# Optimization experiments

Hardware: AMD Instinct MI355X
Metric: run time of the kernel (lower is better)

The kernel has to match this reference:

```python
import jax, jax.numpy as jnp
import numpy as np

T, BLOCK, SIG = 4096, 1024, 1024
LAM = 0.25


def _lstm_cell(x, h, c, Wih, Whh, bih, bhh):
    # PyTorch LSTM gate order: i, f, g, o
    gates = x @ Wih.T + h @ Whh.T + bih + bhh  # [1, 4H]
    i, f, g, o = jnp.split(gates, 4, axis=-1)
    i = jax.nn.sigmoid(i)
    f = jax.nn.sigmoid(f)
    g = jnp.tanh(g)
    o = jax.nn.sigmoid(o)
    c_new = f * c + i * g
    h_new = o * jnp.tanh(c_new)
    return h_new, c_new


def setup_inputs() -> dict:
    key = jax.random.key(0)
    ks = jax.random.split(key, 9)
    ke = 1.0 / np.sqrt(SIG)
    kd = 1.0 / np.sqrt(BLOCK)
    inputs = jax.random.normal(ks[0], (T, 1, BLOCK), dtype=jnp.float32)
    enc_Wih = jax.random.uniform(ks[1], (4 * SIG, BLOCK), jnp.float32, -ke, ke)
    enc_Whh = jax.random.uniform(ks[2], (4 * SIG, SIG), jnp.float32, -ke, ke)
    enc_bih = jax.random.uniform(ks[3], (4 * SIG,), jnp.float32, -ke, ke)
    enc_bhh = jax.random.uniform(ks[4], (4 * SIG,), jnp.float32, -ke, ke)
    dec_Wih = jax.random.uniform(ks[5], (4 * BLOCK, SIG), jnp.float32, -kd, kd)
    dec_Whh = jax.random.uniform(ks[6], (4 * BLOCK, BLOCK), jnp.float32, -kd, kd)
    dec_bih = jax.random.uniform(ks[7], (4 * BLOCK,), jnp.float32, -kd, kd)
    dec_bhh = jax.random.uniform(ks[8], (4 * BLOCK,), jnp.float32, -kd, kd)
    return {"inputs": inputs, "enc_Wih": enc_Wih, "enc_Whh": enc_Whh,
            "enc_bih": enc_bih, "enc_bhh": enc_bhh, "dec_Wih": dec_Wih,
            "dec_Whh": dec_Whh, "dec_bih": dec_bih, "dec_bhh": dec_bhh}


def reference(inputs, enc_Wih, enc_Whh, enc_bih, enc_bhh,
              dec_Wih, dec_Whh, dec_bih, dec_bhh):
    H = enc_Whh.shape[1]
    B = inputs.shape[-1]

    # encode: full-sequence LSTM, zero initial state, batch=1
    def enc_step(carry, x):
        h, c = carry
        h, c = _lstm_cell(x, h, c, enc_Wih, enc_Whh, enc_bih, enc_bhh)
        return (h, c), h

    h0 = jnp.zeros((1, H), inputs.dtype)
    c0 = jnp.zeros((1, H), inputs.dtype)
    _, signal = jax.lax.scan(enc_step, (h0, c0), inputs)  # [T, 1, H]

    # decode: one LSTM step per i; h0 reset to inputs[i], cell state carried
    def dec_step(c, xs):
        x, h_init = xs  # x = signal[i+1], h_init = inputs[i]
        h, c = _lstm_cell(x, h_init, c, dec_Wih, dec_Whh, dec_bih, dec_bhh)
        return c, h

    cdec0 = jnp.zeros((1, B), inputs.dtype)
    _, decoded = jax.lax.scan(dec_step, cdec0, (signal[1:], inputs[:-1]))  # [T-1, 1, B]

    target = inputs[1:]
    mse_loss = jnp.mean((decoded - target) ** 2)
    l1_reg = jnp.sum(jnp.abs(signal)) / signal.size
    loss = mse_loss + LAM * l1_reg
    return loss, mse_loss, l1_reg
```

## Files before the change

kernel.cpp:

```cpp
#include <hip/hip_runtime.h>
#include <math.h>

#define TSTEPS 4096
#define DIM 1024
#define GDIM 4096
#define ENC_NB 64
#define NREP 8
#define NSEG 64
#define SEGLEN 64

typedef short bf16x8 __attribute__((ext_vector_type(8)));
typedef float f32x4 __attribute__((ext_vector_type(4)));
typedef unsigned int uint4v __attribute__((ext_vector_type(4)));

__device__ __forceinline__ float sigmoidf_(float x) {
    return 1.0f / (1.0f + expf(-x));
}

__device__ __forceinline__ void loadcvt(const float* __restrict__ p,
                                        bf16x8& hi, bf16x8& lo)
{
    float4 a = *(const float4*)p;
    float4 b = *(const float4*)(p + 4);
    float f[8] = {a.x, a.y, a.z, a.w, b.x, b.y, b.z, b.w};
    uint4v hw, lw;
    #pragma unroll
    for (int j = 0; j < 4; ++j) {
        unsigned u0 = __float_as_uint(f[2*j]);
        unsigned u1 = __float_as_uint(f[2*j+1]);
        unsigned m0 = u0 & 0xffff0000u;
        unsigned m1 = u1 & 0xffff0000u;
        float r0 = f[2*j]   - __uint_as_float(m0);
        float r1 = f[2*j+1] - __uint_as_float(m1);
        hw[j] = __builtin_amdgcn_perm(u1, u0, 0x07060302u);
        lw[j] = __builtin_amdgcn_perm(__float_as_uint(r1), __float_as_uint(r0),
                                      0x07060302u);
    }
    hi = __builtin_bit_cast(bf16x8, hw);
    lo = __builtin_bit_cast(bf16x8, lw);
}

template<bool DUAL>
__global__ __launch_bounds__(256)
void gemm_split(const float* __restrict__ A1, const float* __restrict__ B1,
                const float* __restrict__ A2, const float* __restrict__ B2,
                const float* __restrict__ bias1, const float* __restrict__ bias2,
                float* __restrict__ C, int N)
{
    const int lane = threadIdx.x & 63;
    const int wid  = threadIdx.x >> 6;
    const int m0 = blockIdx.y * 128 + (wid >> 1) * 64;
    const int n0 = blockIdx.x * 128 + (wid & 1) * 64;
    const int rA   = m0 + (lane & 15);
    const int cB   = n0 + (lane & 15);
    const int koff = (lane >> 4) * 8;

    f32x4 acc[4][4] = {};

    const int npass = DUAL ? 2 : 1;
    for (int pass = 0; pass < npass; ++pass) {
        const float* __restrict__ A = (DUAL && pass) ? A2 : A1;
        const float* __restrict__ B = (DUAL && pass) ? B2 : B1;
        for (int k0 = 0; k0 < 1024; k0 += 32) {
            bf16x8 ah[4], al[4], bh[4], bl[4];
            #pragma unroll
            for (int i = 0; i < 4; ++i)
                loadcvt(A + (size_t)(rA + i * 16) * 1024 + k0 + koff, ah[i], al[i]);
            #pragma unroll
            for (int j = 0; j < 4; ++j)
                loadcvt(B + (size_t)(cB + j * 16) * 1024 + k0 + koff, bh[j], bl[j]);
            #pragma unroll
            for (int i = 0; i < 4; ++i)
                #pragma unroll
                for (int j = 0; j < 4; ++j) {
                    acc[i][j] = __builtin_amdgcn_mfma_f32_16x16x32_bf16(
                        ah[i], bh[j], acc[i][j], 0, 0, 0);
                    acc[i][j] = __builtin_amdgcn_mfma_f32_16x16x32_bf16(
                        ah[i], bl[j], acc[i][j], 0, 0, 0);
                    acc[i][j] = __builtin_amdgcn_mfma_f32_16x16x32_bf16(
                        al[i], bh[j], acc[i][j], 0, 0, 0);
                }
        }
    }

    const int er = (lane >> 4) * 4;
    const int ec = lane & 15;
    #pragma unroll
    for (int j = 0; j < 4; ++j) {
        int col = n0 + j * 16 + ec;
        float bb = bias1[col] + bias2[col];
        #pragma unroll
        for (int i = 0; i < 4; ++i) {
            int rowb = m0 + i * 16 + er;
            #pragma unroll
            for (int r = 0; r < 4; ++r)
                C[(size_t)(rowb + r) * N + col] = acc[i][j][r] + bb;
        }
    }
}

__global__ __launch_bounds__(1024)
void encoder_scan(const float* __restrict__ Xg,
                  const float* __restrict__ Whh,
                  float* __restrict__ signal,
                  unsigned long long* __restrict__ reps,
                  float* __restrict__ l1_acc)
{
    const int b = blockIdx.x;
    const int t = threadIdx.x;
    const int hbase = b * 16;
    const int w = t >> 6;
    const int j = t & 63;
    const int q = j >> 4;
    const int sub = j & 15;
    const int ch = hbase + w;
    const int grow = q * 1024 + ch;

    float4 wreg[16];
    {
        const float4* wrow = (const float4*)(Whh + (size_t)grow * 1024 + sub * 64);
        #pragma unroll
        for (int i = 0; i < 16; ++i) wreg[i] = wrow[i];
    }

    __shared__ float hls[2][16 * 68];
    __shared__ float hstage[16];

    unsigned long long* __restrict__ myrep =
        reps + (size_t)(b & (NREP - 1)) * 2 * 1024;

    float c = 0.f;
    float l1 = 0.f;

    for (int step = 0; step < TSTEPS; ++step) {
        const unsigned us = (unsigned)step;
        float xg = 0.f;
        if (sub == 0) xg = Xg[(size_t)step * GDIM + grow];

        const unsigned long long* sp = myrep + (size_t)(step & 1) * 1024 + t;
        unsigned long long v;
        while (true) {
            v = __hip_atomic_load(sp, __ATOMIC_RELAXED, __HIP_MEMORY_SCOPE_AGENT);
            if ((unsigned)(v >> 32) >= us) break;
            __builtin_amdgcn_s_sleep(1);
        }

        float* hb = hls[step & 1];
        hb[w * 68 + j] = __uint_as_float((unsigned)v);
        __syncthreads();

        float s = 0.f;
        const float* hv = hb + sub * 68;
        #pragma unroll
        for (int i = 0; i < 16; ++i) {
            float4 h4 = *(const float4*)(hv + i * 4);
            s = fmaf(wreg[i].x, h4.x, s); s = fmaf(wreg[i].y, h4.y, s);
            s = fmaf(wreg[i].z, h4.z, s); s = fmaf(wreg[i].w, h4.w, s);
        }
        s += __shfl_xor(s, 1);
        s += __shfl_xor(s, 2);
        s += __shfl_xor(s, 4);
        s += __shfl_xor(s, 8);

        float act = 0.f;
        if (sub == 0) {
            float pre = s + xg;
            act = (q == 2) ? tanhf(pre) : sigmoidf_(pre);
        }
        float fv = __shfl(act, 16);
        float gv = __shfl(act, 32);
        float ov = __shfl(act, 48);
        if (j == 0) {
            c = fmaf(fv, c, act * gv);
            hstage[w] = ov * tanhf(c);
        }
        __syncthreads();

        if (t < 16 * NREP) {
            const int rr = t >> 4, i = t & 15;
            float h = hstage[i];
            unsigned long long pv =
                ((unsigned long long)(us + 1) << 32) | __float_as_uint(h);
            __hip_atomic_store(
                reps + ((size_t)rr * 2 + ((step + 1) & 1)) * 1024 + hbase + i,
                pv, __ATOMIC_RELAXED, __HIP_MEMORY_SCOPE_AGENT);
            if (t < 16) {
                signal[(size_t)step * DIM + hbase + t] = h;
                l1 += fabsf(h);
            }
        }
    }
    if (t < 16) {
        #pragma unroll
        for (int off = 8; off >= 1; off >>= 1) l1 += __shfl_xor(l1, off);
        if (t == 0) atomicAdd(l1_acc, l1);
    }
}

__global__ __launch_bounds__(256)
void dec_compose(const float* __restrict__ G, float* __restrict__ Aseg,
                 float* __restrict__ Bseg)
{
    const int j = blockIdx.x * 256 + threadIdx.x;
    const int s = blockIdx.y;
    const int t0 = s * SEGLEN;
    const int t1 = min(t0 + SEGLEN, TSTEPS - 1);
    float A = 1.f, Bv = 0.f;
    for (int t = t0; t < t1; ++t) {
        const float* g = G + (size_t)t * GDIM;
        float iv = sigmoidf_(g[j]);
        float fv = sigmoidf_(g[j + 1024]);
        float gv = tanhf(g[j + 2048]);
        A *= fv;
        Bv = fmaf(fv, Bv, iv * gv);
    }
    Aseg[s * DIM + j] = A;
    Bseg[s * DIM + j] = Bv;
}

__global__ __launch_bounds__(1024)
void dec_scan(const float* __restrict__ Aseg, const float* __restrict__ Bseg,
              float* __restrict__ cinit)
{
    const int j = threadIdx.x;
    float c = 0.f;
    for (int s = 0; s < NSEG; ++s) {
        cinit[s * DIM + j] = c;
        c = fmaf(Aseg[s * DIM + j], c, Bseg[s * DIM + j]);
    }
}

__global__ __launch_bounds__(256)
void dec_emit(const float* __restrict__ G, const float* __restrict__ inp,
              const float* __restrict__ cinit, float* __restrict__ mse_acc)
{
    const int j = blockIdx.x * 256 + threadIdx.x;
    const int s = blockIdx.y;
    const int t0 = s * SEGLEN;
    const int t1 = min(t0 + SEGLEN, TSTEPS - 1);
    float c = cinit[s * DIM + j];
    float acc = 0.f;
    for (int t = t0; t < t1; ++t) {
        const float* g = G + (size_t)t * GDIM;
        float iv = sigmoidf_(g[j]);
        float fv = sigmoidf_(g[j + 1024]);
        float gv = tanhf(g[j + 2048]);
        float ov = sigmoidf_(g[j + 3072]);
        c = fmaf(fv, c, iv * gv);
        float d = ov * tanhf(c);
        float diff = d - inp[(size_t)(t + 1) * DIM + j];
        acc = fmaf(diff, diff, acc);
    }
    #pragma unroll
    for (int off = 32; off >= 1; off >>= 1) acc += __shfl_xor(acc, off);
    if ((threadIdx.x & 63) == 0) atomicAdd(mse_acc, acc);
}

__global__ void finalize(const float* __restrict__ scal, float* __restrict__ out)
{
    float mse = scal[0] / ((float)(TSTEPS - 1) * (float)DIM);
    float l1  = scal[1] / ((float)TSTEPS * (float)DIM);
    out[0] = mse + 0.25f * l1;
    out[1] = mse;
    out[2] = l1;
}

extern "C" void kernel_launch(void* const* d_in, const int* in_sizes, int n_in,
                              void* d_out, int out_size, void* d_ws, size_t ws_size,
                              hipStream_t stream)
{
    const float* inputs  = (const float*)d_in[0];
    const float* enc_Wih = (const float*)d_in[1];
    const float* enc_Whh = (const float*)d_in[2];
    const float* enc_bih = (const float*)d_in[3];
    const float* enc_bhh = (const float*)d_in[4];
    const float* dec_Wih = (const float*)d_in[5];
    const float* dec_Whh = (const float*)d_in[6];
    const float* dec_bih = (const float*)d_in[7];
    const float* dec_bhh = (const float*)d_in[8];
    float* out = (float*)d_out;

    float* ws = (float*)d_ws;
    float* gates  = ws;
    float* signal = ws + (size_t)16777216;
    unsigned long long* reps =
        (unsigned long long*)(ws + (size_t)20972544);
    float* scal   = ws + (size_t)21005312;
    float* Aseg   = signal;
    float* Bseg   = signal + (size_t)65536;
    float* cinit  = signal + (size_t)131072;
    float* mse_acc = scal + 0;
    float* l1_acc  = scal + 1;

    hipMemsetAsync(ws + (size_t)20971520, 0, (size_t)(1024 + 32768 + 8) * 4, stream);

    dim3 b256(256);
    gemm_split<false><<<dim3(32, 32), b256, 0, stream>>>(
        inputs, enc_Wih, nullptr, nullptr, enc_bih, enc_bhh, gates, GDIM);
    encoder_scan<<<dim3(ENC_NB), dim3(1024), 0, stream>>>(
        gates, enc_Whh, signal, reps, l1_acc);
    gemm_split<true><<<dim3(32, 32), b256, 0, stream>>>(
        signal + DIM, dec_Wih, inputs, dec_Whh, dec_bih, dec_bhh, gates, GDIM);
    dec_compose<<<dim3(4, NSEG), b256, 0, stream>>>(gates, Aseg, Bseg);
    dec_scan<<<dim3(1), dim3(1024), 0, stream>>>(Aseg, Bseg, cinit);
    dec_emit<<<dim3(4, NSEG), b256, 0, stream>>>(gates, inputs, cinit, mse_acc);
    finalize<<<dim3(1), dim3(1), 0, stream>>>(scal, out);
}
```

Measured before the change: 8.783 ms.

## Overlap decoder gate GEMM with encoder scan in a persistent fused kernel

The encoder recurrence and the decoder input GEMM are merged into one 256-block persistent kernel. 64 blocks run the serial encoder scan and publish progress flags every 256 steps. The remaining blocks pull 128x128 GEMM tiles from an atomic work queue and wait until the signal rows each tile needs are finished. This hides the decoder GEMM behind the latency-bound scan, at the cost of spin-waiting, a large padded LDS allocation that forces one block per CU, and possible memory contention that slows the critical scan path.

```diff
diff --git a/kernel.cpp b/kernel.cpp
--- a/kernel.cpp
+++ b/kernel.cpp
@@ -17,12 +17,8 @@
     return 1.0f / (1.0f + expf(-x));
 }
 
-__device__ __forceinline__ void loadcvt(const float* __restrict__ p,
-                                        bf16x8& hi, bf16x8& lo)
-{
-    float4 a = *(const float4*)p;
-    float4 b = *(const float4*)(p + 4);
-    float f[8] = {a.x, a.y, a.z, a.w, b.x, b.y, b.z, b.w};
+__device__ __forceinline__ void pack8(const float* f, bf16x8& hi, bf16x8& lo)
+{
     uint4v hw, lw;
     #pragma unroll
     for (int j = 0; j < 4; ++j) {
@@ -40,6 +36,30 @@
     lo = __builtin_bit_cast(bf16x8, lw);
 }
 
+__device__ __forceinline__ void loadcvt(const float* __restrict__ p,
+                                        bf16x8& hi, bf16x8& lo)
+{
+    float4 a = *(const float4*)p;
+    float4 b = *(const float4*)(p + 4);
+    float f[8] = {a.x, a.y, a.z, a.w, b.x, b.y, b.z, b.w};
+    pack8(f, hi, lo);
+}
+
+__device__ __forceinline__ void loadcvt_vis(const float* __restrict__ p,
+                                            bf16x8& hi, bf16x8& lo)
+{
+    float f[8];
+    #pragma unroll
+    for (int i = 0; i < 4; ++i) {
+        unsigned long long u = __hip_atomic_load(
+            (const unsigned long long*)p + i, __ATOMIC_RELAXED,
+            __HIP_MEMORY_SCOPE_AGENT);
+        float2 f2 = __builtin_bit_cast(float2, u);
+        f[2*i] = f2.x; f[2*i+1] = f2.y;
+    }
+    pack8(f, hi, lo);
+}
+
 template<bool DUAL>
 __global__ __launch_bounds__(256)
 void gemm_split(const float* __restrict__ A1, const float* __restrict__ B1,
@@ -100,100 +120,200 @@
 }
 
 __global__ __launch_bounds__(1024)
-void encoder_scan(const float* __restrict__ Xg,
-                  const float* __restrict__ Whh,
-                  float* __restrict__ signal,
-                  unsigned long long* __restrict__ reps,
-                  float* __restrict__ l1_acc)
-{
-    const int b = blockIdx.x;
-    const int t = threadIdx.x;
-    const int hbase = b * 16;
-    const int w = t >> 6;
-    const int j = t & 63;
-    const int q = j >> 4;
-    const int sub = j & 15;
-    const int ch = hbase + w;
-    const int grow = q * 1024 + ch;
-
-    float4 wreg[16];
-    {
-        const float4* wrow = (const float4*)(Whh + (size_t)grow * 1024 + sub * 64);
-        #pragma unroll
-        for (int i = 0; i < 16; ++i) wreg[i] = wrow[i];
-    }
-
-    __shared__ float hls[2][16 * 68];
-    __shared__ float hstage[16];
-
-    unsigned long long* __restrict__ myrep =
-        reps + (size_t)(b & (NREP - 1)) * 2 * 1024;
-
-    float c = 0.f;
-    float l1 = 0.f;
-
-    for (int step = 0; step < TSTEPS; ++step) {
-        const unsigned us = (unsigned)step;
-        float xg = 0.f;
-        if (sub == 0) xg = Xg[(size_t)step * GDIM + grow];
-
-        const unsigned long long* sp = myrep + (size_t)(step & 1) * 1024 + t;
-        unsigned long long v;
-        while (true) {
-            v = __hip_atomic_load(sp, __ATOMIC_RELAXED, __HIP_MEMORY_SCOPE_AGENT);
-            if ((unsigned)(v >> 32) >= us) break;
-            __builtin_amdgcn_s_sleep(1);
-        }
-
-        float* hb = hls[step & 1];
-        hb[w * 68 + j] = __uint_as_float((unsigned)v);
-        __syncthreads();
-
-        float s = 0.f;
-        const float* hv = hb + sub * 68;
-        #pragma unroll
-        for (int i = 0; i < 16; ++i) {
-            float4 h4 = *(const float4*)(hv + i * 4);
-            s = fmaf(wreg[i].x, h4.x, s); s = fmaf(wreg[i].y, h4.y, s);
-            s = fmaf(wreg[i].z, h4.z, s); s = fmaf(wreg[i].w, h4.w, s);
-        }
-        s += __shfl_xor(s, 1);
-        s += __shfl_xor(s, 2);
-        s += __shfl_xor(s, 4);
-        s += __shfl_xor(s, 8);
-
-        float act = 0.f;
-        if (sub == 0) {
-            float pre = s + xg;
-            act = (q == 2) ? tanhf(pre) : sigmoidf_(pre);
-        }
-        float fv = __shfl(act, 16);
-        float gv = __shfl(act, 32);
-        float ov = __shfl(act, 48);
-        if (j == 0) {
-            c = fmaf(fv, c, act * gv);
-            hstage[w] = ov * tanhf(c);
-        }
-        __syncthreads();
-
-        if (t < 16 * NREP) {
-            const int rr = t >> 4, i = t & 15;
-            float h = hstage[i];
-            unsigned long long pv =
-                ((unsigned long long)(us + 1) << 32) | __float_as_uint(h);
-            __hip_atomic_store(
-                reps + ((size_t)rr * 2 + ((step + 1) & 1)) * 1024 + hbase + i,
-                pv, __ATOMIC_RELAXED, __HIP_MEMORY_SCOPE_AGENT);
-            if (t < 16) {
-                signal[(size_t)step * DIM + hbase + t] = h;
-                l1 += fabsf(h);
-            }
-        }
-    }
-    if (t < 16) {
-        #pragma unroll
-        for (int off = 8; off >= 1; off >>= 1) l1 += __shfl_xor(l1, off);
-        if (t == 0) atomicAdd(l1_acc, l1);
+void mega_scan_gemm(const float* __restrict__ Xg,
+                    const float* __restrict__ Whh,
+                    float* __restrict__ signal,
+                    unsigned long long* __restrict__ reps,
+                    float* __restrict__ l1_acc,
+                    unsigned* __restrict__ flags,
+                    const float* __restrict__ dWih, const float* __restrict__ dWhh,
+                    const float* __restrict__ dbih, const float* __restrict__ dbhh,
+                    const float* __restrict__ inputs,
+                    float* __restrict__ gates,
+                    unsigned* __restrict__ queue)
+{
+    __shared__ float lds_pad_[18432];
+    if ((int)blockDim.y == 7) lds_pad_[threadIdx.x] = 0.f;
+
+    if (blockIdx.x < ENC_NB) {
+        const int b = blockIdx.x;
+        const int t = threadIdx.x;
+        const int hbase = b * 16;
+        const int w = t >> 6;
+        const int j = t & 63;
+        const int q = j >> 4;
+        const int sub = j & 15;
+        const int ch = hbase + w;
+        const int grow = q * 1024 + ch;
+
+        float4 wreg[16];
+        {
+            const float4* wrow = (const float4*)(Whh + (size_t)grow * 1024 + sub * 64);
+            #pragma unroll
+            for (int i = 0; i < 16; ++i) wreg[i] = wrow[i];
+        }
+
+        __shared__ float hls[2][16 * 68];
+        __shared__ float hstage[16];
+
+        unsigned long long* __restrict__ myrep =
+            reps + (size_t)(b & (NREP - 1)) * 2 * 1024;
+
+        float c = 0.f;
+        float l1 = 0.f;
+
+        for (int step = 0; step < TSTEPS; ++step) {
+            const unsigned us = (unsigned)step;
+            float xg = 0.f;
+            if (sub == 0) xg = Xg[(size_t)step * GDIM + grow];
+
+            const unsigned long long* sp = myrep + (size_t)(step & 1) * 1024 + t;
+            unsigned long long v;
+            while (true) {
+                v = __hip_atomic_load(sp, __ATOMIC_RELAXED, __HIP_MEMORY_SCOPE_AGENT);
+                if ((unsigned)(v >> 32) >= us) break;
+                __builtin_amdgcn_s_sleep(1);
+            }
+
+            float* hb = hls[step & 1];
+            hb[w * 68 + j] = __uint_as_float((unsigned)v);
+            __syncthreads();
+
+            float s = 0.f;
+            const float* hv = hb + sub * 68;
+            #pragma unroll
+            for (int i = 0; i < 16; ++i) {
+                float4 h4 = *(const float4*)(hv + i * 4);
+                s = fmaf(wreg[i].x, h4.x, s); s = fmaf(wreg[i].y, h4.y, s);
+                s = fmaf(wreg[i].z, h4.z, s); s = fmaf(wreg[i].w, h4.w, s);
+            }
+            s += __shfl_xor(s, 1);
+            s += __shfl_xor(s, 2);
+            s += __shfl_xor(s, 4);
+            s += __shfl_xor(s, 8);
+
+            float act = 0.f;
+            if (sub == 0) {
+                float pre = s + xg;
+                act = (q == 2) ? tanhf(pre) : sigmoidf_(pre);
+            }
+            float fv = __shfl(act, 16);
+            float gv = __shfl(act, 32);
+            float ov = __shfl(act, 48);
+            if (j == 0) {
+                c = fmaf(fv, c, act * gv);
+                hstage[w] = ov * tanhf(c);
+            }
+            __syncthreads();
+
+            if (t < 16 * NREP) {
+                const int rr = t >> 4, i = t & 15;
+                float h = hstage[i];
+                unsigned long long pv =
+                    ((unsigned long long)(us + 1) << 32) | __float_as_uint(h);
+                __hip_atomic_store(
+                    reps + ((size_t)rr * 2 + ((step + 1) & 1)) * 1024 + hbase + i,
+                    pv, __ATOMIC_RELAXED, __HIP_MEMORY_SCOPE_AGENT);
+                if (t < 16) {
+                    __hip_atomic_store(&signal[(size_t)step * DIM + hbase + t], h,
+                                       __ATOMIC_RELAXED, __HIP_MEMORY_SCOPE_AGENT);
+                    l1 += fabsf(h);
+                    if ((step & 255) == 255) {
+                        __hip_atomic_store(flags + hbase + t, us + 1,
+                                           __ATOMIC_RELEASE, __HIP_MEMORY_SCOPE_AGENT);
+                    }
+                }
+            }
+        }
+        if (t < 16) {
+            #pragma unroll
+            for (int off = 8; off >= 1; off >>= 1) l1 += __shfl_xor(l1, off);
+            if (t == 0) atomicAdd(l1_acc, l1);
+        }
+    } else {
+        const int tid  = threadIdx.x;
+        const int wave = tid >> 6, lane = tid & 63;
+        const int wm = (wave >> 2) * 32, wn = (wave & 3) * 32;
+        const int r16 = lane & 15, koff = (lane >> 4) * 8;
+        __shared__ unsigned s_qi;
+
+        for (;;) {
+            if (tid == 0) s_qi = atomicAdd(queue, 1u);
+            __syncthreads();
+            const unsigned qi = s_qi;
+            __syncthreads();
+            if (qi >= 1024u) break;
+            const int m0 = (int)(qi >> 5) * 128;
+            const int n0 = (int)(qi & 31) * 128;
+
+            {
+                const unsigned need = (unsigned)min(m0 + 129, TSTEPS);
+                if (wave == 0) {
+                    while (true) {
+                        unsigned mn = 0xffffffffu;
+                        #pragma unroll
+                        for (int k2 = 0; k2 < 16; ++k2) {
+                            unsigned f = __hip_atomic_load(
+                                flags + lane * 16 + k2, __ATOMIC_ACQUIRE,
+                                __HIP_MEMORY_SCOPE_AGENT);
+                            mn = min(mn, f);
+                        }
+                        #pragma unroll
+                        for (int off = 32; off >= 1; off >>= 1)
+                            mn = min(mn, (unsigned)__shfl_xor((int)mn, off));
+                        if (mn >= need) break;
+                        __builtin_amdgcn_s_sleep(16);
+                    }
+                }
+                __syncthreads();
+            }
+
+            f32x4 acc[2][2] = {};
+            #pragma unroll
+            for (int pass = 0; pass < 2; ++pass) {
+                const float* __restrict__ A = pass ? inputs : (signal + DIM);
+                const float* __restrict__ B = pass ? dWhh : dWih;
+                for (int k0 = 0; k0 < 1024; k0 += 32) {
+                    bf16x8 ah[2], al[2], bh[2], bl[2];
+                    #pragma unroll
+                    for (int i = 0; i < 2; ++i) {
+                        const float* ap =
+                            A + (size_t)(m0 + wm + i * 16 + r16) * 1024 + k0 + koff;
+                        if (pass == 0) loadcvt_vis(ap, ah[i], al[i]);
+                        else           loadcvt(ap, ah[i], al[i]);
+                    }
+                    #pragma unroll
+                    for (int jj = 0; jj < 2; ++jj)
+                        loadcvt(B + (size_t)(n0 + wn + jj * 16 + r16) * 1024 + k0 + koff,
+                                bh[jj], bl[jj]);
+                    #pragma unroll
+                    for (int i = 0; i < 2; ++i)
+                        #pragma unroll
+                        for (int jj = 0; jj < 2; ++jj) {
+                            acc[i][jj] = __builtin_amdgcn_mfma_f32_16x16x32_bf16(
+                                ah[i], bh[jj], acc[i][jj], 0, 0, 0);
+                            acc[i][jj] = __builtin_amdgcn_mfma_f32_16x16x32_bf16(
+                                ah[i], bl[jj], acc[i][jj], 0, 0, 0);
+                            acc[i][jj] = __builtin_amdgcn_mfma_f32_16x16x32_bf16(
+                                al[i], bh[jj], acc[i][jj], 0, 0, 0);
+                        }
+                }
+            }
+
+            const int er = (lane >> 4) * 4, ec = lane & 15;
+            #pragma unroll
+            for (int jj = 0; jj < 2; ++jj) {
+                int col = n0 + wn + jj * 16 + ec;
+                float bb = dbih[col] + dbhh[col];
+                #pragma unroll
+                for (int i = 0; i < 2; ++i) {
+                    int rowb = m0 + wm + i * 16 + er;
+                    #pragma unroll
+                    for (int r = 0; r < 4; ++r)
+                        gates[(size_t)(rowb + r) * GDIM + col] = acc[i][jj][r] + bb;
+                }
+            }
+        }
     }
 }
 
@@ -286,21 +406,23 @@
     unsigned long long* reps =
         (unsigned long long*)(ws + (size_t)20972544);
     float* scal   = ws + (size_t)21005312;
+    unsigned* flags = (unsigned*)(ws + (size_t)21005320);
+    unsigned* queue = (unsigned*)(ws + (size_t)21006344);
     float* Aseg   = signal;
     float* Bseg   = signal + (size_t)65536;
     float* cinit  = signal + (size_t)131072;
     float* mse_acc = scal + 0;
     float* l1_acc  = scal + 1;
 
-    hipMemsetAsync(ws + (size_t)20971520, 0, (size_t)(1024 + 32768 + 8) * 4, stream);
+    hipMemsetAsync(ws + (size_t)20971520, 0,
+                   (size_t)(1024 + 32768 + 8 + 1024 + 8) * 4, stream);
 
     dim3 b256(256);
     gemm_split<false><<<dim3(32, 32), b256, 0, stream>>>(
         inputs, enc_Wih, nullptr, nullptr, enc_bih, enc_bhh, gates, GDIM);
-    encoder_scan<<<dim3(ENC_NB), dim3(1024), 0, stream>>>(
-        gates, enc_Whh, signal, reps, l1_acc);
-    gemm_split<true><<<dim3(32, 32), b256, 0, stream>>>(
-        signal + DIM, dec_Wih, inputs, dec_Whh, dec_bih, dec_bhh, gates, GDIM);
+    mega_scan_gemm<<<dim3(256), dim3(1024), 0, stream>>>(
+        gates, enc_Whh, signal, reps, l1_acc, flags,
+        dec_Wih, dec_Whh, dec_bih, dec_bhh, inputs, gates, queue);
     dec_compose<<<dim3(4, NSEG), b256, 0, stream>>>(gates, Aseg, Bseg);
     dec_scan<<<dim3(1), dim3(1024), 0, stream>>>(Aseg, Bseg, cinit);
     dec_emit<<<dim3(4, NSEG), b256, 0, stream>>>(gates, inputs, cinit, mse_acc);
```

Result: slower. 15.62 ms (+77.8%).
